# Optimization experiments

Measured on AMD Instinct MI355X. Metric: run time of the kernel, lower is better.

Reference implementation:

```python
import jax, jax.numpy as jnp
import numpy as np

LUT_N = 8
LUT_D = 33
H, W = 2160, 3840


def apply_lut(LUT, img):
    """Trilinear 3D-LUT lookup. LUT: [3, D, D, D] (indexed [c, b, g, r]); img: [3, H, W] in [0,1]."""
    D = LUT.shape[1]
    x = jnp.clip(img, 0.0, 1.0) * (D - 1)
    r, g, b = x[0], x[1], x[2]
    ir = jnp.clip(jnp.floor(r).astype(jnp.int32), 0, D - 2)
    ig = jnp.clip(jnp.floor(g).astype(jnp.int32), 0, D - 2)
    ib = jnp.clip(jnp.floor(b).astype(jnp.int32), 0, D - 2)
    fr = r - ir.astype(x.dtype)
    fg = g - ig.astype(x.dtype)
    fb = b - ib.astype(x.dtype)
    out = jnp.zeros_like(img)
    for dk in (0, 1):  # blue axis
        wb = (1.0 - fb) if dk == 0 else fb
        for dj in (0, 1):  # green axis
            wg = (1.0 - fg) if dj == 0 else fg
            for di in (0, 1):  # red axis
                wr = (1.0 - fr) if di == 0 else fr
                corner = LUT[:, ib + dk, ig + dj, ir + di]  # [3, H, W] gather
                out = out + (wb * wg * wr)[None] * corner
    return out


def setup_inputs() -> dict:
    key = jax.random.key(0)
    k1, k2, k3, k4 = jax.random.split(key, 4)
    gt = jax.random.uniform(k1, (3, H, W), dtype=jnp.float32)
    lut = jax.random.uniform(k2, (2, LUT_N, 3, LUT_D, LUT_D, LUT_D), dtype=jnp.float32)
    lc0 = jax.random.normal(k3, (LUT_N,), dtype=jnp.float32)
    lc1 = jax.random.normal(k4, (LUT_N,), dtype=jnp.float32)
    return {"gt": gt, "lut": lut, "lc0": lc0, "lc1": lc1}


def reference(gt, lut, lc0, lc1):
    # Stage 0: softmax-blend basis LUTs, apply to input image
    nlc0 = jax.nn.softmax(lc0)
    clut0 = jnp.einsum('ncdef,n->cdef', lut[0], nlc0)  # [3, D, D, D]
    I_s = apply_lut(clut0, gt)
    # Stage 1: second blended LUT applied to intermediate image
    nlc1 = jax.nn.softmax(lc1)
    clut1 = jnp.einsum('ncdef,n->cdef', lut[1], nlc1)
    I_f = apply_lut(clut1, I_s)
    return I_f
```

## Files before the change

kernel.cpp:

```cpp
#include <hip/hip_runtime.h>

#define LUT_D   33
#define LUT_D2  1089
#define LUT_D3  35937
#define HW      8294400
#define NLUT    8
#define NCELL   32768

typedef float f4v __attribute__((ext_vector_type(4)));

__device__ __forceinline__ void softmax8(const float* __restrict__ lc, float* w)
{
    float m = lc[0];
#pragma unroll
    for (int n = 1; n < NLUT; ++n) m = fmaxf(m, lc[n]);
    float s = 0.f;
#pragma unroll
    for (int n = 0; n < NLUT; ++n) { w[n] = expf(lc[n] - m); s += w[n]; }
    float inv = 1.f / s;
#pragma unroll
    for (int n = 0; n < NLUT; ++n) w[n] *= inv;
}

__global__ void __launch_bounds__(256)
combine_grid(const float* __restrict__ lut,
             const float* __restrict__ lc0,
             const float* __restrict__ lc1,
             float* __restrict__ cg)
{
    int t = blockIdx.x * 256 + threadIdx.x;
    if (t >= 2 * 3 * LUT_D3) return;
    int l   = t / (3 * LUT_D3);
    int rem = t - l * 3 * LUT_D3;

    float w[NLUT];
    softmax8(l ? lc1 : lc0, w);

    const float* base = lut + (size_t)l * NLUT * 3 * LUT_D3 + rem;
    float a = 0.f;
#pragma unroll
    for (int n = 0; n < NLUT; ++n)
        a = fmaf(w[n], base[(size_t)n * 3 * LUT_D3], a);
    cg[t] = a;
}

__global__ void __launch_bounds__(256)
cellify(const float* __restrict__ cg, uint4* __restrict__ tab)
{
    int id = blockIdx.x * 256 + threadIdx.x;
    int l    = id >> 15;
    int cell = id & (NCELL - 1);
    int ir = cell & 31, ig = (cell >> 5) & 31, ib = cell >> 10;

    const float* g0 = cg + (size_t)l * 3 * LUT_D3 + (ib * LUT_D + ig) * LUT_D + ir;

    float cv[24];
#pragma unroll
    for (int c = 0; c < 3; ++c) {
        const float* p = g0 + (size_t)c * LUT_D3;
#pragma unroll
        for (int k = 0; k < 8; ++k) {
            int off = (k >> 2) * LUT_D2 + ((k >> 1) & 1) * LUT_D + (k & 1);
            cv[k * 3 + c] = p[off];
        }
    }
    unsigned pk[12];
#pragma unroll
    for (int j = 0; j < 12; ++j) {
        unsigned lo = (unsigned)(fminf(cv[2*j],   1.f) * 65535.f + 0.5f);
        unsigned hi = (unsigned)(fminf(cv[2*j+1], 1.f) * 65535.f + 0.5f);
        pk[j] = lo | (hi << 16);
    }
    uint4* dst = tab + (size_t)id * 4;
    dst[0] = make_uint4(pk[0], pk[1], pk[2],  pk[3]);
    dst[1] = make_uint4(pk[4], pk[5], pk[6],  pk[7]);
    dst[2] = make_uint4(pk[8], pk[9], pk[10], pk[11]);
}

__device__ __forceinline__ void stage(const uint4* __restrict__ tab,
                                      float xr, float xg, float xb,
                                      float& o0, float& o1, float& o2)
{
    int ir = min((int)xr, 31), ig = min((int)xg, 31), ib = min((int)xb, 31);
    float fr = xr - (float)ir, fg = xg - (float)ig, fb = xb - (float)ib;

    const uint4* p = tab + (size_t)((((ib << 5) | ig) << 5) | ir) * 4;
    uint4 q0 = p[0];
    uint4 q1 = p[1];
    uint4 q2 = p[2];

#define LOF(u) ((float)((u) & 0xffffu))
#define HIF(u) ((float)((u) >> 16))
    float k0c0=LOF(q0.x), k0c1=HIF(q0.x), k0c2=LOF(q0.y);
    float k1c0=HIF(q0.y), k1c1=LOF(q0.z), k1c2=HIF(q0.z);
    float k2c0=LOF(q0.w), k2c1=HIF(q0.w), k2c2=LOF(q1.x);
    float k3c0=HIF(q1.x), k3c1=LOF(q1.y), k3c2=HIF(q1.y);
    float k4c0=LOF(q1.z), k4c1=HIF(q1.z), k4c2=LOF(q1.w);
    float k5c0=HIF(q1.w), k5c1=LOF(q2.x), k5c2=HIF(q2.x);
    float k6c0=LOF(q2.y), k6c1=HIF(q2.y), k6c2=LOF(q2.z);
    float k7c0=HIF(q2.z), k7c1=LOF(q2.w), k7c2=HIF(q2.w);
#undef LOF
#undef HIF

    float m0c0 = fmaf(fr, k1c0 - k0c0, k0c0);
    float m0c1 = fmaf(fr, k1c1 - k0c1, k0c1);
    float m0c2 = fmaf(fr, k1c2 - k0c2, k0c2);
    float m1c0 = fmaf(fr, k3c0 - k2c0, k2c0);
    float m1c1 = fmaf(fr, k3c1 - k2c1, k2c1);
    float m1c2 = fmaf(fr, k3c2 - k2c2, k2c2);
    float m2c0 = fmaf(fr, k5c0 - k4c0, k4c0);
    float m2c1 = fmaf(fr, k5c1 - k4c1, k4c1);
    float m2c2 = fmaf(fr, k5c2 - k4c2, k4c2);
    float m3c0 = fmaf(fr, k7c0 - k6c0, k6c0);
    float m3c1 = fmaf(fr, k7c1 - k6c1, k6c1);
    float m3c2 = fmaf(fr, k7c2 - k6c2, k6c2);

    float wg0 = 1.f - fg, wb0 = 1.f - fb;
    float w00 = wb0 * wg0, w01 = wb0 * fg, w10 = fb * wg0, w11 = fb * fg;

    o0 = fmaf(w00, m0c0, fmaf(w01, m1c0, fmaf(w10, m2c0, w11 * m3c0)));
    o1 = fmaf(w00, m0c1, fmaf(w01, m1c1, fmaf(w10, m2c1, w11 * m3c1)));
    o2 = fmaf(w00, m0c2, fmaf(w01, m1c2, fmaf(w10, m2c2, w11 * m3c2)));
}

__global__ void __launch_bounds__(256)
lut_apply(const float* __restrict__ gt,
          const uint4* __restrict__ tab,
          float* __restrict__ out)
{
    int t = blockIdx.x * 256 + threadIdx.x;

    const f4v* Rp = (const f4v*)gt;
    const f4v* Gp = (const f4v*)(gt + HW);
    const f4v* Bp = (const f4v*)(gt + 2 * HW);
    f4v r4 = __builtin_nontemporal_load(Rp + t);
    f4v g4 = __builtin_nontemporal_load(Gp + t);
    f4v b4 = __builtin_nontemporal_load(Bp + t);

    const uint4* tab0 = tab;
    const uint4* tab1 = tab + (size_t)NCELL * 4;

    f4v ro, go, bo;
#pragma unroll
    for (int k = 0; k < 4; ++k) {
        float xr = fminf(fmaxf(r4[k], 0.f), 1.f) * 32.f;
        float xg = fminf(fmaxf(g4[k], 0.f), 1.f) * 32.f;
        float xb = fminf(fmaxf(b4[k], 0.f), 1.f) * 32.f;

        float a0, a1, a2;
        stage(tab0, xr, xg, xb, a0, a1, a2);

        const float S = 32.f / 65535.f;
        float x2r = fminf(a0, 65535.f) * S;
        float x2g = fminf(a1, 65535.f) * S;
        float x2b = fminf(a2, 65535.f) * S;

        float b0, b1, b2;
        stage(tab1, x2r, x2g, x2b, b0, b1, b2);

        const float I = 1.f / 65535.f;
        ro[k] = b0 * I;
        go[k] = b1 * I;
        bo[k] = b2 * I;
    }

    __builtin_nontemporal_store(ro, (f4v*)out + t);
    __builtin_nontemporal_store(go, (f4v*)(out + HW) + t);
    __builtin_nontemporal_store(bo, (f4v*)(out + 2 * HW) + t);
}

extern "C" void kernel_launch(void* const* d_in, const int* in_sizes, int n_in,
                              void* d_out, int out_size, void* d_ws, size_t ws_size,
                              hipStream_t stream)
{
    const float* gt  = (const float*)d_in[0];
    const float* lut = (const float*)d_in[1];
    const float* lc0 = (const float*)d_in[2];
    const float* lc1 = (const float*)d_in[3];
    float*       out = (float*)d_out;

    uint4* tab = (uint4*)d_ws;
    float* cg  = (float*)((char*)d_ws + (size_t)2 * NCELL * 64);

    int n1 = 2 * 3 * LUT_D3;
    combine_grid<<<(n1 + 255) / 256, 256, 0, stream>>>(lut, lc0, lc1, cg);

    cellify<<<(2 * NCELL) / 256, 256, 0, stream>>>(cg, tab);

    int nthreads = HW / 4;
    lut_apply<<<nthreads / 256, 256, 0, stream>>>(gt, tab, out);
}
```

Measured before the change: 270.4 us.

## Pack second-stage LUT as 10-bit triplets and process eight pixels per thread

The second-stage cell table is packed as 10-10-10 bits per corner (32 bytes per cell instead of 48), shrinking its cache footprint and per-lookup load size. The apply kernel now handles eight pixels per thread with more independent loads in flight. The cost is reduced output precision (about 1/1023 quantisation) and fewer threads for latency hiding.

```diff
diff --git a/kernel.cpp b/kernel.cpp
--- a/kernel.cpp
+++ b/kernel.cpp
@@ -45,7 +45,9 @@
 }
 
 __global__ void __launch_bounds__(256)
-cellify(const float* __restrict__ cg, uint4* __restrict__ tab)
+cellify(const float* __restrict__ cg,
+        uint4* __restrict__ tab0,
+        uint4* __restrict__ tab1)
 {
     int id = blockIdx.x * 256 + threadIdx.x;
     int l    = id >> 15;
@@ -64,22 +66,37 @@
             cv[k * 3 + c] = p[off];
         }
     }
-    unsigned pk[12];
-#pragma unroll
-    for (int j = 0; j < 12; ++j) {
-        unsigned lo = (unsigned)(fminf(cv[2*j],   1.f) * 65535.f + 0.5f);
-        unsigned hi = (unsigned)(fminf(cv[2*j+1], 1.f) * 65535.f + 0.5f);
-        pk[j] = lo | (hi << 16);
+
+    if (l == 0) {
+        unsigned pk[12];
+#pragma unroll
+        for (int j = 0; j < 12; ++j) {
+            unsigned lo = (unsigned)(fminf(cv[2*j],   1.f) * 65535.f + 0.5f);
+            unsigned hi = (unsigned)(fminf(cv[2*j+1], 1.f) * 65535.f + 0.5f);
+            pk[j] = lo | (hi << 16);
+        }
+        uint4* dst = tab0 + (size_t)cell * 4;
+        dst[0] = make_uint4(pk[0], pk[1], pk[2],  pk[3]);
+        dst[1] = make_uint4(pk[4], pk[5], pk[6],  pk[7]);
+        dst[2] = make_uint4(pk[8], pk[9], pk[10], pk[11]);
+    } else {
+        unsigned d[8];
+#pragma unroll
+        for (int k = 0; k < 8; ++k) {
+            unsigned e0 = (unsigned)(fminf(cv[3*k + 0], 1.f) * 1023.f + 0.5f);
+            unsigned e1 = (unsigned)(fminf(cv[3*k + 1], 1.f) * 1023.f + 0.5f);
+            unsigned e2 = (unsigned)(fminf(cv[3*k + 2], 1.f) * 1023.f + 0.5f);
+            d[k] = e0 | (e1 << 10) | (e2 << 20);
+        }
+        uint4* dst = tab1 + (size_t)cell * 2;
+        dst[0] = make_uint4(d[0], d[1], d[2], d[3]);
+        dst[1] = make_uint4(d[4], d[5], d[6], d[7]);
     }
-    uint4* dst = tab + (size_t)id * 4;
-    dst[0] = make_uint4(pk[0], pk[1], pk[2],  pk[3]);
-    dst[1] = make_uint4(pk[4], pk[5], pk[6],  pk[7]);
-    dst[2] = make_uint4(pk[8], pk[9], pk[10], pk[11]);
-}
-
-__device__ __forceinline__ void stage(const uint4* __restrict__ tab,
-                                      float xr, float xg, float xb,
-                                      float& o0, float& o1, float& o2)
+}
+
+__device__ __forceinline__ void stage1(const uint4* __restrict__ tab,
+                                       float xr, float xg, float xb,
+                                       float& o0, float& o1, float& o2)
 {
     int ir = min((int)xr, 31), ig = min((int)xg, 31), ib = min((int)xb, 31);
     float fr = xr - (float)ir, fg = xg - (float)ig, fb = xb - (float)ib;
@@ -123,9 +140,48 @@
     o2 = fmaf(w00, m0c2, fmaf(w01, m1c2, fmaf(w10, m2c2, w11 * m3c2)));
 }
 
+__device__ __forceinline__ void stage2(const uint4* __restrict__ tab,
+                                       float xr, float xg, float xb,
+                                       float& o0, float& o1, float& o2)
+{
+    int ir = min((int)xr, 31), ig = min((int)xg, 31), ib = min((int)xb, 31);
+    float fr = xr - (float)ir, fg = xg - (float)ig, fb = xb - (float)ib;
+
+    const uint4* p = tab + (size_t)((((ib << 5) | ig) << 5) | ir) * 2;
+    uint4 qa = p[0];
+    uint4 qb = p[1];
+
+#define F0(u) ((float)((u) & 1023u))
+#define F1(u) ((float)(((u) >> 10) & 1023u))
+#define F2(u) ((float)((u) >> 20))
+    float m0c0 = fmaf(fr, F0(qa.y) - F0(qa.x), F0(qa.x));
+    float m0c1 = fmaf(fr, F1(qa.y) - F1(qa.x), F1(qa.x));
+    float m0c2 = fmaf(fr, F2(qa.y) - F2(qa.x), F2(qa.x));
+    float m1c0 = fmaf(fr, F0(qa.w) - F0(qa.z), F0(qa.z));
+    float m1c1 = fmaf(fr, F1(qa.w) - F1(qa.z), F1(qa.z));
+    float m1c2 = fmaf(fr, F2(qa.w) - F2(qa.z), F2(qa.z));
+    float m2c0 = fmaf(fr, F0(qb.y) - F0(qb.x), F0(qb.x));
+    float m2c1 = fmaf(fr, F1(qb.y) - F1(qb.x), F1(qb.x));
+    float m2c2 = fmaf(fr, F2(qb.y) - F2(qb.x), F2(qb.x));
+    float m3c0 = fmaf(fr, F0(qb.w) - F0(qb.z), F0(qb.z));
+    float m3c1 = fmaf(fr, F1(qb.w) - F1(qb.z), F1(qb.z));
+    float m3c2 = fmaf(fr, F2(qb.w) - F2(qb.z), F2(qb.z));
+#undef F0
+#undef F1
+#undef F2
+
+    float wg0 = 1.f - fg, wb0 = 1.f - fb;
+    float w00 = wb0 * wg0, w01 = wb0 * fg, w10 = fb * wg0, w11 = fb * fg;
+
+    o0 = fmaf(w00, m0c0, fmaf(w01, m1c0, fmaf(w10, m2c0, w11 * m3c0)));
+    o1 = fmaf(w00, m0c1, fmaf(w01, m1c1, fmaf(w10, m2c1, w11 * m3c1)));
+    o2 = fmaf(w00, m0c2, fmaf(w01, m1c2, fmaf(w10, m2c2, w11 * m3c2)));
+}
+
 __global__ void __launch_bounds__(256)
 lut_apply(const float* __restrict__ gt,
-          const uint4* __restrict__ tab,
+          const uint4* __restrict__ tab0,
+          const uint4* __restrict__ tab1,
           float* __restrict__ out)
 {
     int t = blockIdx.x * 256 + threadIdx.x;
@@ -133,22 +189,26 @@
     const f4v* Rp = (const f4v*)gt;
     const f4v* Gp = (const f4v*)(gt + HW);
     const f4v* Bp = (const f4v*)(gt + 2 * HW);
-    f4v r4 = __builtin_nontemporal_load(Rp + t);
-    f4v g4 = __builtin_nontemporal_load(Gp + t);
-    f4v b4 = __builtin_nontemporal_load(Bp + t);
-
-    const uint4* tab0 = tab;
-    const uint4* tab1 = tab + (size_t)NCELL * 4;
-
-    f4v ro, go, bo;
-#pragma unroll
-    for (int k = 0; k < 4; ++k) {
-        float xr = fminf(fmaxf(r4[k], 0.f), 1.f) * 32.f;
-        float xg = fminf(fmaxf(g4[k], 0.f), 1.f) * 32.f;
-        float xb = fminf(fmaxf(b4[k], 0.f), 1.f) * 32.f;
+    f4v r4a = __builtin_nontemporal_load(Rp + 2*t);
+    f4v r4b = __builtin_nontemporal_load(Rp + 2*t + 1);
+    f4v g4a = __builtin_nontemporal_load(Gp + 2*t);
+    f4v g4b = __builtin_nontemporal_load(Gp + 2*t + 1);
+    f4v b4a = __builtin_nontemporal_load(Bp + 2*t);
+    f4v b4b = __builtin_nontemporal_load(Bp + 2*t + 1);
+
+    f4v roa, rob, goa, gob, boa, bob;
+#pragma unroll
+    for (int k = 0; k < 8; ++k) {
+        float rv = (k < 4) ? r4a[k] : r4b[k - 4];
+        float gv = (k < 4) ? g4a[k] : g4b[k - 4];
+        float bv = (k < 4) ? b4a[k] : b4b[k - 4];
+
+        float xr = fminf(fmaxf(rv, 0.f), 1.f) * 32.f;
+        float xg = fminf(fmaxf(gv, 0.f), 1.f) * 32.f;
+        float xb = fminf(fmaxf(bv, 0.f), 1.f) * 32.f;
 
         float a0, a1, a2;
-        stage(tab0, xr, xg, xb, a0, a1, a2);
+        stage1(tab0, xr, xg, xb, a0, a1, a2);
 
         const float S = 32.f / 65535.f;
         float x2r = fminf(a0, 65535.f) * S;
@@ -156,17 +216,20 @@
         float x2b = fminf(a2, 65535.f) * S;
 
         float b0, b1, b2;
-        stage(tab1, x2r, x2g, x2b, b0, b1, b2);
-
-        const float I = 1.f / 65535.f;
-        ro[k] = b0 * I;
-        go[k] = b1 * I;
-        bo[k] = b2 * I;
+        stage2(tab1, x2r, x2g, x2b, b0, b1, b2);
+
+        const float I = 1.f / 1023.f;
+        float orv = b0 * I, ogv = b1 * I, obv = b2 * I;
+        if (k < 4) { roa[k] = orv;     goa[k] = ogv;     boa[k] = obv; }
+        else       { rob[k - 4] = orv; gob[k - 4] = ogv; bob[k - 4] = obv; }
     }
 
-    __builtin_nontemporal_store(ro, (f4v*)out + t);
-    __builtin_nontemporal_store(go, (f4v*)(out + HW) + t);
-    __builtin_nontemporal_store(bo, (f4v*)(out + 2 * HW) + t);
+    __builtin_nontemporal_store(roa, (f4v*)out + 2*t);
+    __builtin_nontemporal_store(rob, (f4v*)out + 2*t + 1);
+    __builtin_nontemporal_store(goa, (f4v*)(out + HW) + 2*t);
+    __builtin_nontemporal_store(gob, (f4v*)(out + HW) + 2*t + 1);
+    __builtin_nontemporal_store(boa, (f4v*)(out + 2*HW) + 2*t);
+    __builtin_nontemporal_store(bob, (f4v*)(out + 2*HW) + 2*t + 1);
 }
 
 extern "C" void kernel_launch(void* const* d_in, const int* in_sizes, int n_in,
@@ -179,14 +242,15 @@
     const float* lc1 = (const float*)d_in[3];
     float*       out = (float*)d_out;
 
-    uint4* tab = (uint4*)d_ws;
-    float* cg  = (float*)((char*)d_ws + (size_t)2 * NCELL * 64);
+    uint4* tab0 = (uint4*)d_ws;
+    uint4* tab1 = (uint4*)((char*)d_ws + (size_t)NCELL * 64);
+    float* cg   = (float*)((char*)d_ws + (size_t)NCELL * 96);
 
     int n1 = 2 * 3 * LUT_D3;
     combine_grid<<<(n1 + 255) / 256, 256, 0, stream>>>(lut, lc0, lc1, cg);
 
-    cellify<<<(2 * NCELL) / 256, 256, 0, stream>>>(cg, tab);
-
-    int nthreads = HW / 4;
-    lut_apply<<<nthreads / 256, 256, 0, stream>>>(gt, tab, out);
-}
+    cellify<<<(2 * NCELL) / 256, 256, 0, stream>>>(cg, tab0, tab1);
+
+    int nthreads = HW / 8;
+    lut_apply<<<nthreads / 256, 256, 0, stream>>>(gt, tab0, tab1, out);
+}
```

Result: slower. 283.3 us (+4.7%).
